# Performance work log

Hardware: AMD Instinct MI355X
Metric: run time of the kernel (lower is better)

## Reference

```python
import jax, jax.numpy as jnp
import numpy as np

B, TIN, IN, TRI, D, FFN, L, OUT = 8, 1040, 80, 128, 512, 2048, 8, 1024
H, DH, STRIDE, SEG, RC, LC, MAXMEM = 8, 64, 4, 16, 4, 32, 4
NEG = -1e8
SCALE = DH ** -0.5


def _layer_norm(x, g, b, eps=1e-5):
    m = jnp.mean(x, -1, keepdims=True)
    v = jnp.var(x, -1, keepdims=True)
    return (x - m) * jax.lax.rsqrt(v + eps) * g + b


def _build_attention_mask(U, nseg):
    # Faithful port of Emformer._gen_attention_mask; True = masked out.
    rct = RC * nseg
    mlen = nseg - 1
    rc_rows, q_rows, s_rows = [], [], []
    for i in range(nseg):
        rs, re = i * RC, i * RC + RC
        ss, se = max(i * SEG - LC, 0), min((i + 1) * SEG, U)
        ms = max(i - MAXMEM, 0)
        widths = [ms, i - ms, mlen - i, rs, RC, rct - re, ss, se - ss, U - se]

        def row(allowed):
            return np.concatenate([np.full(max(w, 0), j in allowed, dtype=bool)
                                   for j, w in enumerate(widths)])

        r = row({1, 4, 7})  # memory, own rc block, own (left-extended) segment
        rc_rows.append(np.tile(r, (RC, 1)))
        q_rows.append(np.tile(r, (min(SEG, U - i * SEG), 1)))
        s_rows.append(row({4, 7})[None])  # summary: rc block + segment only
    allow = np.concatenate([np.concatenate(rc_rows), np.concatenate(q_rows), np.concatenate(s_rows)])
    return jnp.asarray(~allow)


def _forward(input, lengths, w_in, ln_in_g, ln_in_b, wq, bq, wk, bk, wv, bv, wo, bo,
             ff_ln_g, ff_ln_b, w1, b1, w2, b2, ln_out_g, ln_out_b, w_out, b_out, lng, lnb):
    x = input @ w_in                                    # (B, TIN, TRI) input_linear (no bias)
    nb, t, _ = x.shape
    nf = t - t % STRIDE
    x = x[:, :nf].reshape(nb, nf // STRIDE, TRI * STRIDE)  # time reduction -> (B, Tr, D)
    lr = lengths // STRIDE
    x = jnp.transpose(x, (1, 0, 2))                     # (Tr, B, D) time-major like torch Emformer
    Tr = x.shape[0]
    U = Tr - RC                                         # utterance length (256)
    nseg = -(-U // SEG)
    utt = x[:U]
    # right-context blocks: hard-copied per segment (last block = trailing rc)
    starts = np.concatenate([np.arange(1, nseg) * SEG, [Tr - RC]])
    idx = (starts[:, None] + np.arange(RC)[None, :]).reshape(-1)
    rc = x[idx]                                         # (nseg*RC, B, D)
    Rt = rc.shape[0]
    Q = Rt + U + nseg                                   # rc + utterance + summary queries
    K = (nseg - 1) + Rt + U                             # mems + rc + utterance keys
    attn_mask = _build_attention_mask(U, nseg)          # (Q, K)
    mems0 = utt.reshape(nseg, SEG, nb, D).mean(1)[:-1]  # AvgPool1d(seg) on raw utterance, drop last
    # padding mask over keys (faithful to _gen_padding_mask)
    rcbl = Q - jnp.max(lr) - nseg
    klen = lr + (nseg - 1) + rcbl
    pad = jnp.arange(K)[None, :] >= klen[:, None]       # (B, K), True = masked

    def step(carry, p):
        utt, rc, mems = carry
        g1, be1, Wq, Bq, Wk, Bk, Wv, Bv, Wo, Bo, g2, be2, Wf1, Bf1, Wf2, Bf2, g3, be3 = p
        ln = _layer_norm(jnp.concatenate([rc, utt]), g1, be1)
        ln_rc, ln_utt = ln[:Rt], ln[Rt:]
        summary = ln_utt.reshape(nseg, SEG, nb, D).mean(1)       # (nseg, B, D)
        qin = jnp.concatenate([ln_rc, ln_utt, summary])          # (Q, B, D)
        kin = jnp.concatenate([mems, ln_rc, ln_utt])             # (K, B, D)
        q = (qin @ Wq + Bq).reshape(Q, nb, H, DH)
        k = (kin @ Wk + Bk).reshape(K, nb, H, DH)
        v = (kin @ Wv + Bv).reshape(K, nb, H, DH)
        w = jnp.einsum('qbhd,kbhd->bhqk', q * SCALE, k)
        w = jnp.where(attn_mask[None, None], NEG, w)
        w = jnp.where(pad[:, None, None, :], NEG, w)
        probs = jax.nn.softmax(w, axis=-1)
        att = jnp.einsum('bhqk,kbhd->qbhd', probs, v).reshape(Q, nb, D)
        out = att @ Wo + Bo
        rcu = out[:Rt + U]
        new_mems = jnp.tanh(out[Rt + U:])[:-1]                   # tanh_on_mem=True, drop last summary
        res = rcu + jnp.concatenate([rc, utt])                   # residual w/ pre-LN input
        h = _layer_norm(res, g2, be2)
        h = jax.nn.relu(h @ Wf1 + Bf1) @ Wf2 + Bf2               # pos_ff (pre-LN inside)
        res = res + h
        res = _layer_norm(res, g3, be3)
        return (res[Rt:], res[:Rt], new_mems), None

    xs = (ln_in_g, ln_in_b, wq, bq, wk, bk, wv, bv, wo, bo,
          ff_ln_g, ff_ln_b, w1, b1, w2, b2, ln_out_g, ln_out_b)
    (utt, rc, mems), _ = jax.lax.scan(step, (utt, rc, mems0), xs)
    y = jnp.transpose(utt, (1, 0, 2))                   # (B, U, D)
    y = _layer_norm(y @ w_out + b_out, lng, lnb)        # output_linear + LayerNorm
    return y, lr


def setup_inputs() -> dict:
    key = jax.random.key(0)
    ks = jax.random.split(key, 12)

    def w(k, shape, fan):
        return jax.random.normal(k, shape, jnp.float32) / np.sqrt(fan)

    return {
        "input": jax.random.normal(ks[0], (B, TIN, IN), jnp.float32),
        "lengths": jax.random.randint(ks[1], (B,), 256, 1025, jnp.int32),
        "w_in": w(ks[2], (IN, TRI), IN),
        "ln_in_g": jnp.ones((L, D), jnp.float32), "ln_in_b": jnp.zeros((L, D), jnp.float32),
        "wq": w(ks[3], (L, D, D), D), "bq": jnp.zeros((L, D), jnp.float32),
        "wk": w(ks[4], (L, D, D), D), "bk": jnp.zeros((L, D), jnp.float32),
        "wv": w(ks[5], (L, D, D), D), "bv": jnp.zeros((L, D), jnp.float32),
        "wo": w(ks[6], (L, D, D), D), "bo": jnp.zeros((L, D), jnp.float32),
        "ff_ln_g": jnp.ones((L, D), jnp.float32), "ff_ln_b": jnp.zeros((L, D), jnp.float32),
        "w1": w(ks[7], (L, D, FFN), D), "b1": jnp.zeros((L, FFN), jnp.float32),
        "w2": w(ks[8], (L, FFN, D), FFN), "b2": jnp.zeros((L, D), jnp.float32),
        "ln_out_g": jnp.ones((L, D), jnp.float32), "ln_out_b": jnp.zeros((L, D), jnp.float32),
        "w_out": w(ks[9], (D, OUT), D), "b_out": jnp.zeros((OUT,), jnp.float32),
        "lng": jnp.ones((OUT,), jnp.float32), "lnb": jnp.zeros((OUT,), jnp.float32),
    }


def reference(input, lengths, w_in, ln_in_g, ln_in_b, wq, bq, wk, bk, wv, bv, wo, bo,
              ff_ln_g, ff_ln_b, w1, b1, w2, b2, ln_out_g, ln_out_b, w_out, b_out, lng, lnb):
    return _forward(input, lengths, w_in, ln_in_g, ln_in_b, wq, bq, wk, bk, wv, bv, wo, bo,
                    ff_ln_g, ff_ln_b, w1, b1, w2, b2, ln_out_g, ln_out_b, w_out, b_out, lng, lnb)
```

## Files before the change

### kernel.cpp

```cpp
#include <hip/hip_runtime.h>
#include <math.h>

#define NB 8
#define D 512
#define H 8
#define DH 64
#define NSEG 16
#define RT 64
#define UU 256
#define QN 336
#define KN 335
#define SROWS 320
#define FFN_D 2048
#define LAYERS 8
#define OUTD 1024
#define TR 260
#define NEGV (-100000000.0f)
#define QSCALE 0.125f

typedef __attribute__((ext_vector_type(8))) short bf16x8;
typedef __attribute__((ext_vector_type(4))) float f32x4;

__device__ inline unsigned short f2bf(float f) {
    union { float f; unsigned int u; } v; v.f = f;
    unsigned int u = v.u;
    unsigned int r = (u + 0x7FFFu + ((u >> 16) & 1u)) >> 16;
    return (unsigned short)r;
}
__device__ inline float bf2f(unsigned short h) {
    union { unsigned int u; float f; } v; v.u = ((unsigned int)h) << 16;
    return v.f;
}

__global__ void lr_k(const int* __restrict__ lengths, int* __restrict__ lrw,
                     float* __restrict__ out_lr) {
    if (threadIdx.x == 0) {
        int mx = 0;
        for (int b = 0; b < NB; ++b) {
            int v = lengths[b] >> 2;
            lrw[b] = v;
            out_lr[b] = (float)v;
            if (v > mx) mx = v;
        }
        lrw[NB] = mx;
    }
}

__global__ __launch_bounds__(128) void inproj_k(const float* __restrict__ input,
                                                const float* __restrict__ w_in,
                                                float* __restrict__ XB) {
    __shared__ float wl[80 * 128];
    __shared__ float il[4 * 80];
    int tid = threadIdx.x;
    int t = blockIdx.x >> 3;
    int b = blockIdx.x & 7;
    for (int i = tid; i < 80 * 128; i += 128) wl[i] = w_in[i];
    const float* inp = input + ((size_t)b * 1040 + (size_t)t * 4) * 80;
    for (int i = tid; i < 320; i += 128) il[i] = inp[i];
    __syncthreads();
    float* xrow = XB + ((size_t)(t * NB + b)) * D;
#pragma unroll
    for (int c = 0; c < 4; ++c) {
        float acc = 0.f;
        for (int i = 0; i < 80; ++i) acc = fmaf(il[c * 80 + i], wl[i * 128 + tid], acc);
        xrow[c * 128 + tid] = acc;
    }
}

__global__ __launch_bounds__(256) void initstate_k(const float* __restrict__ XB,
                                                   float* __restrict__ S) {
    int r = blockIdx.x;
    int srow = r >> 3, b = r & 7;
    int src;
    if (srow < RT) {
        int i = srow >> 2, jj = srow & 3;
        src = (i < 15 ? (i + 1) * 16 : 256) + jj;
    } else {
        src = srow - RT;
    }
    const float* xr = XB + ((size_t)(src * NB + b)) * D;
    float* sr = S + (size_t)r * D;
    sr[threadIdx.x] = xr[threadIdx.x];
    sr[threadIdx.x + 256] = xr[threadIdx.x + 256];
}

__global__ __launch_bounds__(256) void mems0_k(const float* __restrict__ XB,
                                               unsigned short* __restrict__ MEMS) {
    int ib = blockIdx.x;
    int i = ib >> 3, b = ib & 7;
    for (int c = 0; c < 2; ++c) {
        int col = threadIdx.x + c * 256;
        float s = 0.f;
#pragma unroll
        for (int t = 0; t < 16; ++t) s += XB[((size_t)((i * 16 + t) * NB + b)) * D + col];
        MEMS[(size_t)ib * D + col] = f2bf(s * (1.f / 16.f));
    }
}

__global__ __launch_bounds__(256) void ln_k(const float* __restrict__ X,
                                            unsigned short* __restrict__ Y16,
                                            float* __restrict__ Yf,
                                            const float* __restrict__ g,
                                            const float* __restrict__ be, int dual) {
    int row = blockIdx.x;
    const float* x = X + (size_t)row * D;
    float v[2];
    float s = 0.f, ss = 0.f;
#pragma unroll
    for (int j = 0; j < 2; ++j) {
        v[j] = x[threadIdx.x + j * 256];
        s += v[j];
        ss = fmaf(v[j], v[j], ss);
    }
#pragma unroll
    for (int off = 32; off; off >>= 1) {
        s += __shfl_xor(s, off);
        ss += __shfl_xor(ss, off);
    }
    __shared__ float rs_[4], rss_[4];
    int w = threadIdx.x >> 6;
    if ((threadIdx.x & 63) == 0) {
        rs_[w] = s;
        rss_[w] = ss;
    }
    __syncthreads();
    s = rs_[0] + rs_[1] + rs_[2] + rs_[3];
    ss = rss_[0] + rss_[1] + rss_[2] + rss_[3];
    float mean = s * (1.f / D);
    float var = ss * (1.f / D) - mean * mean;
    float rstd = rsqrtf(var + 1e-5f);
#pragma unroll
    for (int j = 0; j < 2; ++j) {
        int col = threadIdx.x + j * 256;
        float y = (v[j] - mean) * rstd * g[col] + be[col];
        Y16[(size_t)row * D + col] = f2bf(y);
        if (dual) Yf[(size_t)row * D + col] = y;
    }
}

__global__ __launch_bounds__(256) void ln_res_k(const float* __restrict__ OUTB,
                                                float* __restrict__ SB,
                                                unsigned short* __restrict__ MEMS,
                                                unsigned short* __restrict__ Y16,
                                                const float* __restrict__ g,
                                                const float* __restrict__ be) {
    int row = blockIdx.x;
    if (row >= SROWS * NB) {
        int j = row - SROWS * NB;
#pragma unroll
        for (int c = 0; c < 2; ++c) {
            int col = threadIdx.x + c * 256;
            MEMS[(size_t)j * D + col] = f2bf(tanhf(OUTB[(size_t)row * D + col]));
        }
        return;
    }
    float v[2];
    float s = 0.f, ss = 0.f;
#pragma unroll
    for (int j = 0; j < 2; ++j) {
        int col = threadIdx.x + j * 256;
        float r = SB[(size_t)row * D + col] + OUTB[(size_t)row * D + col];
        SB[(size_t)row * D + col] = r;
        v[j] = r;
        s += r;
        ss = fmaf(r, r, ss);
    }
#pragma unroll
    for (int off = 32; off; off >>= 1) {
        s += __shfl_xor(s, off);
        ss += __shfl_xor(ss, off);
    }
    __shared__ float rs_[4], rss_[4];
    int w = threadIdx.x >> 6;
    if ((threadIdx.x & 63) == 0) {
        rs_[w] = s;
        rss_[w] = ss;
    }
    __syncthreads();
    s = rs_[0] + rs_[1] + rs_[2] + rs_[3];
    ss = rss_[0] + rss_[1] + rss_[2] + rss_[3];
    float mean = s * (1.f / D);
    float var = ss * (1.f / D) - mean * mean;
    float rstd = rsqrtf(var + 1e-5f);
#pragma unroll
    for (int j = 0; j < 2; ++j) {
        int col = threadIdx.x + j * 256;
        Y16[(size_t)row * D + col] = f2bf((v[j] - mean) * rstd * g[col] + be[col]);
    }
}

__global__ __launch_bounds__(256) void summary_k(const unsigned short* __restrict__ LN16,
                                                 unsigned short* __restrict__ SUM16) {
    int ib = blockIdx.x;
    int i = ib >> 3, b = ib & 7;
    for (int c = 0; c < 2; ++c) {
        int col = threadIdx.x + c * 256;
        float s = 0.f;
#pragma unroll
        for (int t = 0; t < 16; ++t)
            s += bf2f(LN16[((size_t)((RT + i * 16 + t) * NB + b)) * D + col]);
        SUM16[(size_t)ib * D + col] = f2bf(s * (1.f / 16.f));
    }
}

__device__ inline void conv_tile(float (*tile)[33], const float* __restrict__ src, int srcN,
                                 int k0, int sn0, unsigned short* __restrict__ dst, int dstK,
                                 int dn0) {
    int t = threadIdx.x;
    int r = t >> 3, c4 = (t & 7) * 4;
    float4 v = *(const float4*)&src[(size_t)(k0 + r) * srcN + sn0 + c4];
    tile[r][c4 + 0] = v.x;
    tile[r][c4 + 1] = v.y;
    tile[r][c4 + 2] = v.z;
    tile[r][c4 + 3] = v.w;
    __syncthreads();
    ushort4 o;
    o.x = f2bf(tile[c4 + 0][r]);
    o.y = f2bf(tile[c4 + 1][r]);
    o.z = f2bf(tile[c4 + 2][r]);
    o.w = f2bf(tile[c4 + 3][r]);
    *(ushort4*)&dst[(size_t)(dn0 + r) * dstK + k0 + c4] = o;
}

__global__ __launch_bounds__(256) void convw_k(const float* __restrict__ wq,
                                               const float* __restrict__ wk,
                                               const float* __restrict__ wv,
                                               const float* __restrict__ wo,
                                               const float* __restrict__ w1,
                                               const float* __restrict__ w2,
                                               const float* __restrict__ bq,
                                               const float* __restrict__ bk,
                                               const float* __restrict__ bv,
                                               unsigned short* __restrict__ WQKV,
                                               unsigned short* __restrict__ WO16,
                                               unsigned short* __restrict__ W1T,
                                               unsigned short* __restrict__ W2T,
                                               float* __restrict__ BQKV, int l) {
    __shared__ float tile[32][33];
    int t = blockIdx.x;
    if (t == 0) {
        for (int i = threadIdx.x; i < 1536; i += 256)
            BQKV[i] = i < 512 ? bq[l * 512 + i]
                              : (i < 1024 ? bk[l * 512 + i - 512] : bv[l * 512 + i - 1024]);
    }
    if (t < 768) {
        int tn = t % 48, tk = t / 48;
        int n0 = tn * 32, k0 = tk * 32;
        const float* src;
        int sn0;
        if (n0 < 512) { src = wq + (size_t)l * 262144; sn0 = n0; }
        else if (n0 < 1024) { src = wk + (size_t)l * 262144; sn0 = n0 - 512; }
        else { src = wv + (size_t)l * 262144; sn0 = n0 - 1024; }
        conv_tile(tile, src, 512, k0, sn0, WQKV, 512, n0);
    } else if (t < 1024) {
        int tt = t - 768;
        int n0 = (tt % 16) * 32, k0 = (tt / 16) * 32;
        conv_tile(tile, wo + (size_t)l * 262144, 512, k0, n0, WO16, 512, n0);
    } else if (t < 2048) {
        int tt = t - 1024;
        int n0 = (tt % 64) * 32, k0 = (tt / 64) * 32;
        conv_tile(tile, w1 + (size_t)l * 1048576, 2048, k0, n0, W1T, 512, n0);
    } else {
        int tt = t - 2048;
        int n0 = (tt % 16) * 32, k0 = (tt / 16) * 32;
        conv_tile(tile, w2 + (size_t)l * 1048576, 512, k0, n0, W2T, 2048, n0);
    }
}

__global__ __launch_bounds__(256) void convout_k(const float* __restrict__ w_out,
                                                 unsigned short* __restrict__ WOUT16) {
    __shared__ float tile[32][33];
    int t = blockIdx.x;
    int n0 = (t % 32) * 32, k0 = (t / 32) * 32;
    conv_tile(tile, w_out, 1024, k0, n0, WOUT16, 512, n0);
}

__global__ __launch_bounds__(256) void gemm16_k(const unsigned short* __restrict__ A,
                                                const unsigned short* __restrict__ BT,
                                                const float* __restrict__ bias,
                                                void* __restrict__ Cp, int M, int N, int K,
                                                int Kchunk, int flags) {
    __shared__ unsigned short As[2][64][40];
    __shared__ unsigned short Bs[2][64][40];
    int tid = threadIdx.x;
    int wave = tid >> 6, lane = tid & 63;
    int wm = wave >> 1, wn = wave & 1;
    int quad = lane >> 4, sub = lane & 15;
    int m0 = blockIdx.y * 64, n0 = blockIdx.x * 64;
    int kb = blockIdx.z * Kchunk, ke = kb + Kchunk;

    int lrow = tid >> 3, lkc = tid & 7;
    int lrow2 = lrow + 32;
    int lkh = lkc >> 2, lkl = lkc & 3;

    f32x4 acc[2][2] = {};
    int4 ar0, ar1, br0, br1;

    auto loadT = [&](int k0) {
        int gr0 = m0 + lrow, gr1 = m0 + lrow2;
        ar0 = (gr0 < M) ? *(const int4*)&A[(size_t)gr0 * K + k0 + lkc * 8] : make_int4(0, 0, 0, 0);
        ar1 = (gr1 < M) ? *(const int4*)&A[(size_t)gr1 * K + k0 + lkc * 8] : make_int4(0, 0, 0, 0);
        br0 = *(const int4*)&BT[(size_t)(n0 + lrow) * K + k0 + lkc * 8];
        br1 = *(const int4*)&BT[(size_t)(n0 + lrow2) * K + k0 + lkc * 8];
    };
    auto storeT = [&]() {
        *(int4*)&As[lkh][lrow][lkl * 8] = ar0;
        *(int4*)&As[lkh][lrow2][lkl * 8] = ar1;
        *(int4*)&Bs[lkh][lrow][lkl * 8] = br0;
        *(int4*)&Bs[lkh][lrow2][lkl * 8] = br1;
    };
    auto compute = [&]() {
#pragma unroll
        for (int ks = 0; ks < 2; ++ks) {
            bf16x8 af[2], bf[2];
#pragma unroll
            for (int mi = 0; mi < 2; ++mi)
                af[mi] = *(const bf16x8*)&As[ks][wm * 32 + mi * 16 + sub][quad * 8];
#pragma unroll
            for (int ni = 0; ni < 2; ++ni)
                bf[ni] = *(const bf16x8*)&Bs[ks][wn * 32 + ni * 16 + sub][quad * 8];
#pragma unroll
            for (int mi = 0; mi < 2; ++mi)
#pragma unroll
                for (int ni = 0; ni < 2; ++ni)
                    acc[mi][ni] = __builtin_amdgcn_mfma_f32_16x16x32_bf16(af[mi], bf[ni],
                                                                          acc[mi][ni], 0, 0, 0);
        }
    };

    loadT(kb);
    storeT();
    __syncthreads();
    for (int k0 = kb + 64; k0 < ke; k0 += 64) {
        loadT(k0);
        compute();
        __syncthreads();
        storeT();
        __syncthreads();
    }
    compute();

    bool relu = flags & 1, addc = flags & 2, obf = flags & 4, atom = flags & 8;
    bool addbias = !atom || blockIdx.z == 0;
    float* Cf = (float*)Cp;
    unsigned short* Ch = (unsigned short*)Cp;
#pragma unroll
    for (int mi = 0; mi < 2; ++mi) {
#pragma unroll
        for (int ni = 0; ni < 2; ++ni) {
#pragma unroll
            for (int r = 0; r < 4; ++r) {
                int row = m0 + wm * 32 + mi * 16 + quad * 4 + r;
                int col = n0 + wn * 32 + ni * 16 + sub;
                if (row < M) {
                    float v = acc[mi][ni][r] + (addbias ? bias[col] : 0.f);
                    if (relu) v = fmaxf(v, 0.f);
                    size_t idx = (size_t)row * N + col;
                    if (obf) {
                        Ch[idx] = f2bf(v);
                    } else if (atom) {
                        atomicAdd(&Cf[idx], v);
                    } else {
                        if (addc) v += Cf[idx];
                        Cf[idx] = v;
                    }
                }
            }
        }
    }
}

__global__ __launch_bounds__(256) void attn_k(const unsigned short* __restrict__ QKV,
                                              unsigned short* __restrict__ ATT,
                                              const int* __restrict__ lrw) {
    int tid = threadIdx.x;
    int qrow = blockIdx.x;
    int b = blockIdx.y;

    int i, is_sum;
    if (qrow < RT) {
        i = qrow >> 2;
        is_sum = 0;
    } else if (qrow < RT + UU) {
        i = (qrow - RT) >> 4;
        is_sum = 0;
    } else {
        i = qrow - (RT + UU);
        is_sum = 1;
    }
    int ms = (i > 4) ? (i - 4) : 0;
    int n_mem = is_sum ? 0 : (i - ms);
    int us = (i * 16 - 32 > 0) ? (i * 16 - 32) : 0;
    int ue = (i + 1) * 16;
    int total = n_mem + 4 + (ue - us);
    int klen = KN + lrw[b] - lrw[NB];

    __shared__ float qs[512];
    __shared__ float sc[H][64];
    __shared__ int kks[64];

    {
        const unsigned int* qrp =
            (const unsigned int*)&QKV[(size_t)(120 + qrow * NB + b) * 1536];
        unsigned int u = qrp[tid];
        qs[2 * tid] = __uint_as_float(u << 16) * QSCALE;
        qs[2 * tid + 1] = __uint_as_float(u & 0xFFFF0000u) * QSCALE;
    }
    if (tid < 64) {
        int kk = -1;
        if (tid < total) {
            if (tid < n_mem)
                kk = ms + tid;
            else if (tid < n_mem + 4)
                kk = 15 + i * 4 + (tid - n_mem);
            else
                kk = 79 + us + (tid - n_mem - 4);
        }
        kks[tid] = kk;
    }
    __syncthreads();

#pragma unroll
    for (int rep = 0; rep < 2; ++rep) {
        int p = rep * 256 + tid;
        int h = p >> 6, j = p & 63;
        int kk = kks[j];
        float s = NEGV;
        if (kk >= 0 && kk < klen) {
            const int4* kr = (const int4*)&QKV[(size_t)(kk * NB + b) * 1536 + 512 + h * DH];
            const float* qh = &qs[h * DH];
            float accd = 0.f;
#pragma unroll
            for (int c = 0; c < 8; ++c) {
                int4 kv = kr[c];
                const int uu[4] = {kv.x, kv.y, kv.z, kv.w};
#pragma unroll
                for (int jj = 0; jj < 4; ++jj) {
                    float lo = __uint_as_float(((unsigned)uu[jj]) << 16);
                    float hi = __uint_as_float(((unsigned)uu[jj]) & 0xFFFF0000u);
                    accd = fmaf(lo, qh[c * 8 + jj * 2], accd);
                    accd = fmaf(hi, qh[c * 8 + jj * 2 + 1], accd);
                }
            }
            s = accd;
        }
        sc[h][j] = s;
    }
    __syncthreads();

    {
        int wv = tid >> 6, lane = tid & 63;
#pragma unroll
        for (int hh = 0; hh < 2; ++hh) {
            int h = wv + hh * 4;
            float s = sc[h][lane];
            float m = s;
#pragma unroll
            for (int off = 32; off; off >>= 1) m = fmaxf(m, __shfl_xor(m, off));
            float p = __expf(s - m);
            float sum = p;
#pragma unroll
            for (int off = 32; off; off >>= 1) sum += __shfl_xor(sum, off);
            sc[h][lane] = p / sum;
        }
    }
    __syncthreads();

    {
        int h = tid >> 5;
        const float* ph = sc[h];
        float a0 = 0.f, a1 = 0.f;
        const unsigned short* vbase = QKV + (size_t)b * 1536 + 1024 + 2 * tid;
#pragma unroll 4
        for (int j = 0; j < total; ++j) {
            int kkj = kks[j];
            unsigned int u = *(const unsigned int*)&vbase[(size_t)kkj * (NB * 1536)];
            float p = ph[j];
            a0 = fmaf(p, __uint_as_float(u << 16), a0);
            a1 = fmaf(p, __uint_as_float(u & 0xFFFF0000u), a1);
        }
        unsigned int o = ((unsigned int)f2bf(a0)) | (((unsigned int)f2bf(a1)) << 16);
        *(unsigned int*)&ATT[(size_t)(qrow * NB + b) * D + 2 * tid] = o;
    }
}

__global__ __launch_bounds__(256) void final_ln_k(const float* __restrict__ Yb,
                                                  const float* __restrict__ g,
                                                  const float* __restrict__ be,
                                                  float* __restrict__ out) {
    int row = blockIdx.x;
    int u = row >> 3, b = row & 7;
    const float* x = Yb + (size_t)row * OUTD;
    float v[4];
    float s = 0.f, ss = 0.f;
#pragma unroll
    for (int j = 0; j < 4; ++j) {
        v[j] = x[threadIdx.x + j * 256];
        s += v[j];
        ss = fmaf(v[j], v[j], ss);
    }
#pragma unroll
    for (int off = 32; off; off >>= 1) {
        s += __shfl_xor(s, off);
        ss += __shfl_xor(ss, off);
    }
    __shared__ float rs_[4], rss_[4];
    int w = threadIdx.x >> 6;
    if ((threadIdx.x & 63) == 0) {
        rs_[w] = s;
        rss_[w] = ss;
    }
    __syncthreads();
    s = rs_[0] + rs_[1] + rs_[2] + rs_[3];
    ss = rss_[0] + rss_[1] + rss_[2] + rss_[3];
    float mean = s * (1.f / OUTD);
    float var = ss * (1.f / OUTD) - mean * mean;
    float rstd = rsqrtf(var + 1e-5f);
    float* o = out + ((size_t)(b * 256 + u)) * OUTD;
#pragma unroll
    for (int j = 0; j < 4; ++j) {
        int col = threadIdx.x + j * 256;
        o[col] = (v[j] - mean) * rstd * g[col] + be[col];
    }
}

extern "C" void kernel_launch(void* const* d_in, const int* in_sizes, int n_in, void* d_out,
                              int out_size, void* d_ws, size_t ws_size, hipStream_t stream) {
    (void)in_sizes;
    (void)n_in;
    (void)out_size;
    (void)ws_size;
    const float* input = (const float*)d_in[0];
    const int* lengths = (const int*)d_in[1];
    const float* w_in = (const float*)d_in[2];
    const float* ln_in_g = (const float*)d_in[3];
    const float* ln_in_b = (const float*)d_in[4];
    const float* wq = (const float*)d_in[5];
    const float* bq = (const float*)d_in[6];
    const float* wk = (const float*)d_in[7];
    const float* bk = (const float*)d_in[8];
    const float* wv = (const float*)d_in[9];
    const float* bv = (const float*)d_in[10];
    const float* wo = (const float*)d_in[11];
    const float* bo = (const float*)d_in[12];
    const float* ff_g = (const float*)d_in[13];
    const float* ff_b = (const float*)d_in[14];
    const float* w1 = (const float*)d_in[15];
    const float* b1 = (const float*)d_in[16];
    const float* w2 = (const float*)d_in[17];
    const float* b2 = (const float*)d_in[18];
    const float* lo_g = (const float*)d_in[19];
    const float* lo_b = (const float*)d_in[20];
    const float* w_out = (const float*)d_in[21];
    const float* b_out = (const float*)d_in[22];
    const float* lng = (const float*)d_in[23];
    const float* lnb = (const float*)d_in[24];
    float* out = (float*)d_out;

    char* wsc = (char*)d_ws;
    size_t off = 0;
    auto alloc = [&](size_t bytes) {
        char* p = wsc + off;
        off += (bytes + 255) & ~(size_t)255;
        return p;
    };
    unsigned short* ACT16 = (unsigned short*)alloc(2808ULL * 512 * 2);
    unsigned short* ATT16 = (unsigned short*)alloc(2688ULL * 512 * 2);
    unsigned short* HB16 = (unsigned short*)alloc(2560ULL * 2048 * 2);
    unsigned short* QKVB = (unsigned short*)alloc(2808ULL * 1536 * 2);
    float* SB = (float*)alloc(2560ULL * 512 * 4);
    unsigned short* WQKV16 = (unsigned short*)alloc(1536ULL * 512 * 2);
    unsigned short* WO16 = (unsigned short*)alloc(512ULL * 512 * 2);
    unsigned short* W1T = (unsigned short*)alloc(2048ULL * 512 * 2);
    unsigned short* W2T = (unsigned short*)alloc(512ULL * 2048 * 2);
    unsigned short* WOUT16 = (unsigned short*)alloc(1024ULL * 512 * 2);
    float* BQKV = (float*)alloc(1536 * 4);
    int* LRW = (int*)alloc(64);

    unsigned short* MEMS16 = ACT16;
    unsigned short* LNB16 = ACT16 + 120 * 512;
    unsigned short* SUMB16 = ACT16 + 2680 * 512;
    float* XB = (float*)QKVB;
    float* OUTB = (float*)QKVB;
    float* HBf = (float*)QKVB;

    lr_k<<<1, 64, 0, stream>>>(lengths, LRW, out + (size_t)NB * 256 * 1024);
    convout_k<<<512, 256, 0, stream>>>(w_out, WOUT16);
    inproj_k<<<TR * NB, 128, 0, stream>>>(input, w_in, XB);
    initstate_k<<<SROWS * NB, 256, 0, stream>>>(XB, SB);
    mems0_k<<<15 * NB, 256, 0, stream>>>(XB, MEMS16);

    for (int l = 0; l < LAYERS; ++l) {
        convw_k<<<3072, 256, 0, stream>>>(wq, wk, wv, wo, w1, w2, bq, bk, bv, WQKV16, WO16, W1T,
                                          W2T, BQKV, l);
        ln_k<<<SROWS * NB, 256, 0, stream>>>(SB, LNB16, SB, ln_in_g + l * D, ln_in_b + l * D, 0);
        summary_k<<<NSEG * NB, 256, 0, stream>>>(LNB16, SUMB16);
        gemm16_k<<<dim3(24, 44, 1), 256, 0, stream>>>(ACT16, WQKV16, BQKV, QKVB, 2808, 1536, 512,
                                                      512, 4);
        attn_k<<<dim3(QN, NB), 256, 0, stream>>>(QKVB, ATT16, LRW);
        gemm16_k<<<dim3(8, 42, 1), 256, 0, stream>>>(ATT16, WO16, bo + l * D, OUTB, QN * NB, D,
                                                     D, D, 0);
        ln_res_k<<<(SROWS + 15) * NB, 256, 0, stream>>>(OUTB, SB, MEMS16, LNB16, ff_g + l * D,
                                                        ff_b + l * D);
        gemm16_k<<<dim3(32, 40, 1), 256, 0, stream>>>(LNB16, W1T, b1 + l * FFN_D, HB16,
                                                      SROWS * NB, FFN_D, D, D, 1 | 4);
        gemm16_k<<<dim3(8, 40, 4), 256, 0, stream>>>(HB16, W2T, b2 + l * D, SB, SROWS * NB, D,
                                                     FFN_D, 512, 8);
        ln_k<<<SROWS * NB, 256, 0, stream>>>(SB, LNB16, SB, lo_g + l * D, lo_b + l * D, 1);
    }
    gemm16_k<<<dim3(16, 32, 1), 256, 0, stream>>>(LNB16 + (size_t)RT * NB * D, WOUT16, b_out,
                                                  HBf, UU * NB, OUTD, D, D, 0);
    final_ln_k<<<UU * NB, 256, 0, stream>>>(HBf, lng, lnb, out);
}
```

Measured before the change: 1.196 ms.

## Convert all layer weights in one launch and use async LDS loads in GEMM

Moves the per-layer bf16 weight conversion out of the layer loop into a single launch that converts every layer's weights plus the output projection into per-layer buffers, which removes eight serialized conversion launches. The GEMM kernel now copies its A and B tiles straight from global memory into LDS with global_load_lds, into an XOR-swizzled single buffer that avoids bank conflicts. This drops the register-staged double buffer, so global loads no longer overlap the MFMA work, and the row bounds check on A is gone. Out-of-range rows (2808 is not a multiple of 64) now read past the end of the A buffer, and the workspace grows to hold all layers' converted weights.

```diff
diff --git a/kernel.cpp b/kernel.cpp
--- a/kernel.cpp
+++ b/kernel.cpp
@@ -32,6 +32,11 @@
     return v.f;
 }
 
+__device__ inline void async16(const void* g, void* l) {
+    __builtin_amdgcn_global_load_lds((const __attribute__((address_space(1))) void*)g,
+                                     (__attribute__((address_space(3))) void*)l, 16, 0, 0);
+}
+
 __global__ void lr_k(const int* __restrict__ lengths, int* __restrict__ lrw,
                      float* __restrict__ out_lr) {
     if (threadIdx.x == 0) {
@@ -222,26 +227,36 @@
     *(ushort4*)&dst[(size_t)(dn0 + r) * dstK + k0 + c4] = o;
 }
 
-__global__ __launch_bounds__(256) void convw_k(const float* __restrict__ wq,
-                                               const float* __restrict__ wk,
-                                               const float* __restrict__ wv,
-                                               const float* __restrict__ wo,
-                                               const float* __restrict__ w1,
-                                               const float* __restrict__ w2,
-                                               const float* __restrict__ bq,
-                                               const float* __restrict__ bk,
-                                               const float* __restrict__ bv,
-                                               unsigned short* __restrict__ WQKV,
-                                               unsigned short* __restrict__ WO16,
-                                               unsigned short* __restrict__ W1T,
-                                               unsigned short* __restrict__ W2T,
-                                               float* __restrict__ BQKV, int l) {
+__global__ __launch_bounds__(256) void convw_all_k(const float* __restrict__ wq,
+                                                   const float* __restrict__ wk,
+                                                   const float* __restrict__ wv,
+                                                   const float* __restrict__ wo,
+                                                   const float* __restrict__ w1,
+                                                   const float* __restrict__ w2,
+                                                   const float* __restrict__ bq,
+                                                   const float* __restrict__ bk,
+                                                   const float* __restrict__ bv,
+                                                   const float* __restrict__ w_out,
+                                                   unsigned short* __restrict__ WQKV,
+                                                   unsigned short* __restrict__ WO16,
+                                                   unsigned short* __restrict__ W1T,
+                                                   unsigned short* __restrict__ W2T,
+                                                   unsigned short* __restrict__ WOUT16,
+                                                   float* __restrict__ BQKV) {
     __shared__ float tile[32][33];
-    int t = blockIdx.x;
+    int tb = blockIdx.x;
+    if (tb >= LAYERS * 3072) {
+        int t = tb - LAYERS * 3072;
+        int n0 = (t % 32) * 32, k0 = (t / 32) * 32;
+        conv_tile(tile, w_out, 1024, k0, n0, WOUT16, 512, n0);
+        return;
+    }
+    int l = tb / 3072, t = tb % 3072;
     if (t == 0) {
         for (int i = threadIdx.x; i < 1536; i += 256)
-            BQKV[i] = i < 512 ? bq[l * 512 + i]
-                              : (i < 1024 ? bk[l * 512 + i - 512] : bv[l * 512 + i - 1024]);
+            BQKV[l * 1536 + i] = i < 512 ? bq[l * 512 + i]
+                                         : (i < 1024 ? bk[l * 512 + i - 512]
+                                                     : bv[l * 512 + i - 1024]);
     }
     if (t < 768) {
         int tn = t % 48, tk = t / 48;
@@ -251,28 +266,23 @@
         if (n0 < 512) { src = wq + (size_t)l * 262144; sn0 = n0; }
         else if (n0 < 1024) { src = wk + (size_t)l * 262144; sn0 = n0 - 512; }
         else { src = wv + (size_t)l * 262144; sn0 = n0 - 1024; }
-        conv_tile(tile, src, 512, k0, sn0, WQKV, 512, n0);
+        conv_tile(tile, src, 512, k0, sn0, WQKV + (size_t)l * 1536 * 512, 512, n0);
     } else if (t < 1024) {
         int tt = t - 768;
         int n0 = (tt % 16) * 32, k0 = (tt / 16) * 32;
-        conv_tile(tile, wo + (size_t)l * 262144, 512, k0, n0, WO16, 512, n0);
+        conv_tile(tile, wo + (size_t)l * 262144, 512, k0, n0, WO16 + (size_t)l * 512 * 512, 512,
+                  n0);
     } else if (t < 2048) {
         int tt = t - 1024;
         int n0 = (tt % 64) * 32, k0 = (tt / 64) * 32;
-        conv_tile(tile, w1 + (size_t)l * 1048576, 2048, k0, n0, W1T, 512, n0);
+        conv_tile(tile, w1 + (size_t)l * 1048576, 2048, k0, n0, W1T + (size_t)l * 2048 * 512, 512,
+                  n0);
     } else {
         int tt = t - 2048;
         int n0 = (tt % 16) * 32, k0 = (tt / 16) * 32;
-        conv_tile(tile, w2 + (size_t)l * 1048576, 512, k0, n0, W2T, 2048, n0);
-    }
-}
-
-__global__ __launch_bounds__(256) void convout_k(const float* __restrict__ w_out,
-                                                 unsigned short* __restrict__ WOUT16) {
-    __shared__ float tile[32][33];
-    int t = blockIdx.x;
-    int n0 = (t % 32) * 32, k0 = (t / 32) * 32;
-    conv_tile(tile, w_out, 1024, k0, n0, WOUT16, 512, n0);
+        conv_tile(tile, w2 + (size_t)l * 1048576, 512, k0, n0, W2T + (size_t)l * 512 * 2048, 2048,
+                  n0);
+    }
 }
 
 __global__ __launch_bounds__(256) void gemm16_k(const unsigned short* __restrict__ A,
@@ -280,8 +290,8 @@
                                                 const float* __restrict__ bias,
                                                 void* __restrict__ Cp, int M, int N, int K,
                                                 int Kchunk, int flags) {
-    __shared__ unsigned short As[2][64][40];
-    __shared__ unsigned short Bs[2][64][40];
+    __shared__ unsigned short As[64 * 64];
+    __shared__ unsigned short Bs[64 * 64];
     int tid = threadIdx.x;
     int wave = tid >> 6, lane = tid & 63;
     int wm = wave >> 1, wn = wave & 1;
@@ -289,56 +299,44 @@
     int m0 = blockIdx.y * 64, n0 = blockIdx.x * 64;
     int kb = blockIdx.z * Kchunk, ke = kb + Kchunk;
 
-    int lrow = tid >> 3, lkc = tid & 7;
-    int lrow2 = lrow + 32;
-    int lkh = lkc >> 2, lkl = lkc & 3;
+    int s0 = wave * 128 + lane;
+    int s1 = s0 + 64;
+    int r0 = s0 >> 3, c0 = (s0 & 7) ^ (r0 & 7);
+    int r1 = s1 >> 3, c1 = (s1 & 7) ^ (r1 & 7);
+    const unsigned short* gA0 = A + (size_t)(m0 + r0) * K + c0 * 8 + kb;
+    const unsigned short* gA1 = A + (size_t)(m0 + r1) * K + c1 * 8 + kb;
+    const unsigned short* gB0 = BT + (size_t)(n0 + r0) * K + c0 * 8 + kb;
+    const unsigned short* gB1 = BT + (size_t)(n0 + r1) * K + c1 * 8 + kb;
+    unsigned short* lA0 = &As[(wave * 128) * 8];
+    unsigned short* lA1 = &As[(wave * 128 + 64) * 8];
+    unsigned short* lB0 = &Bs[(wave * 128) * 8];
+    unsigned short* lB1 = &Bs[(wave * 128 + 64) * 8];
+
+    int rowA0 = wm * 32 + sub, rowA1 = rowA0 + 16;
+    int rowB0 = wn * 32 + sub, rowB1 = rowB0 + 16;
 
     f32x4 acc[2][2] = {};
-    int4 ar0, ar1, br0, br1;
-
-    auto loadT = [&](int k0) {
-        int gr0 = m0 + lrow, gr1 = m0 + lrow2;
-        ar0 = (gr0 < M) ? *(const int4*)&A[(size_t)gr0 * K + k0 + lkc * 8] : make_int4(0, 0, 0, 0);
-        ar1 = (gr1 < M) ? *(const int4*)&A[(size_t)gr1 * K + k0 + lkc * 8] : make_int4(0, 0, 0, 0);
-        br0 = *(const int4*)&BT[(size_t)(n0 + lrow) * K + k0 + lkc * 8];
-        br1 = *(const int4*)&BT[(size_t)(n0 + lrow2) * K + k0 + lkc * 8];
-    };
-    auto storeT = [&]() {
-        *(int4*)&As[lkh][lrow][lkl * 8] = ar0;
-        *(int4*)&As[lkh][lrow2][lkl * 8] = ar1;
-        *(int4*)&Bs[lkh][lrow][lkl * 8] = br0;
-        *(int4*)&Bs[lkh][lrow2][lkl * 8] = br1;
-    };
-    auto compute = [&]() {
+    for (int k0 = 0; k0 < Kchunk; k0 += 64) {
+        async16(gA0 + k0, lA0);
+        async16(gA1 + k0, lA1);
+        async16(gB0 + k0, lB0);
+        async16(gB1 + k0, lB1);
+        __syncthreads();
 #pragma unroll
         for (int ks = 0; ks < 2; ++ks) {
-            bf16x8 af[2], bf[2];
-#pragma unroll
-            for (int mi = 0; mi < 2; ++mi)
-                af[mi] = *(const bf16x8*)&As[ks][wm * 32 + mi * 16 + sub][quad * 8];
-#pragma unroll
-            for (int ni = 0; ni < 2; ++ni)
-                bf[ni] = *(const bf16x8*)&Bs[ks][wn * 32 + ni * 16 + sub][quad * 8];
-#pragma unroll
-            for (int mi = 0; mi < 2; ++mi)
-#pragma unroll
-                for (int ni = 0; ni < 2; ++ni)
-                    acc[mi][ni] = __builtin_amdgcn_mfma_f32_16x16x32_bf16(af[mi], bf[ni],
-                                                                          acc[mi][ni], 0, 0, 0);
-        }
-    };
-
-    loadT(kb);
-    storeT();
-    __syncthreads();
-    for (int k0 = kb + 64; k0 < ke; k0 += 64) {
-        loadT(k0);
-        compute();
+            int cc = ks * 4 + quad;
+            bf16x8 af0 = *(const bf16x8*)&As[rowA0 * 64 + ((cc ^ (rowA0 & 7)) * 8)];
+            bf16x8 af1 = *(const bf16x8*)&As[rowA1 * 64 + ((cc ^ (rowA1 & 7)) * 8)];
+            bf16x8 bf0 = *(const bf16x8*)&Bs[rowB0 * 64 + ((cc ^ (rowB0 & 7)) * 8)];
+            bf16x8 bf1 = *(const bf16x8*)&Bs[rowB1 * 64 + ((cc ^ (rowB1 & 7)) * 8)];
+            acc[0][0] = __builtin_amdgcn_mfma_f32_16x16x32_bf16(af0, bf0, acc[0][0], 0, 0, 0);
+            acc[0][1] = __builtin_amdgcn_mfma_f32_16x16x32_bf16(af0, bf1, acc[0][1], 0, 0, 0);
+            acc[1][0] = __builtin_amdgcn_mfma_f32_16x16x32_bf16(af1, bf0, acc[1][0], 0, 0, 0);
+            acc[1][1] = __builtin_amdgcn_mfma_f32_16x16x32_bf16(af1, bf1, acc[1][1], 0, 0, 0);
+        }
         __syncthreads();
-        storeT();
-        __syncthreads();
-    }
-    compute();
+    }
+    (void)ke;
 
     bool relu = flags & 1, addc = flags & 2, obf = flags & 4, atom = flags & 8;
     bool addbias = !atom || blockIdx.z == 0;
@@ -569,12 +567,12 @@
     unsigned short* HB16 = (unsigned short*)alloc(2560ULL * 2048 * 2);
     unsigned short* QKVB = (unsigned short*)alloc(2808ULL * 1536 * 2);
     float* SB = (float*)alloc(2560ULL * 512 * 4);
-    unsigned short* WQKV16 = (unsigned short*)alloc(1536ULL * 512 * 2);
-    unsigned short* WO16 = (unsigned short*)alloc(512ULL * 512 * 2);
-    unsigned short* W1T = (unsigned short*)alloc(2048ULL * 512 * 2);
-    unsigned short* W2T = (unsigned short*)alloc(512ULL * 2048 * 2);
+    unsigned short* WQKV16 = (unsigned short*)alloc(8ULL * 1536 * 512 * 2);
+    unsigned short* WO16 = (unsigned short*)alloc(8ULL * 512 * 512 * 2);
+    unsigned short* W1T = (unsigned short*)alloc(8ULL * 2048 * 512 * 2);
+    unsigned short* W2T = (unsigned short*)alloc(8ULL * 512 * 2048 * 2);
     unsigned short* WOUT16 = (unsigned short*)alloc(1024ULL * 512 * 2);
-    float* BQKV = (float*)alloc(1536 * 4);
+    float* BQKV = (float*)alloc(8ULL * 1536 * 4);
     int* LRW = (int*)alloc(64);
 
     unsigned short* MEMS16 = ACT16;
@@ -585,30 +583,33 @@
     float* HBf = (float*)QKVB;
 
     lr_k<<<1, 64, 0, stream>>>(lengths, LRW, out + (size_t)NB * 256 * 1024);
-    convout_k<<<512, 256, 0, stream>>>(w_out, WOUT16);
+    convw_all_k<<<LAYERS * 3072 + 512, 256, 0, stream>>>(wq, wk, wv, wo, w1, w2, bq, bk, bv,
+                                                         w_out, WQKV16, WO16, W1T, W2T, WOUT16,
+                                                         BQKV);
     inproj_k<<<TR * NB, 128, 0, stream>>>(input, w_in, XB);
     initstate_k<<<SROWS * NB, 256, 0, stream>>>(XB, SB);
     mems0_k<<<15 * NB, 256, 0, stream>>>(XB, MEMS16);
 
     for (int l = 0; l < LAYERS; ++l) {
-        convw_k<<<3072, 256, 0, stream>>>(wq, wk, wv, wo, w1, w2, bq, bk, bv, WQKV16, WO16, W1T,
-                                          W2T, BQKV, l);
         ln_k<<<SROWS * NB, 256, 0, stream>>>(SB, LNB16, SB, ln_in_g + l * D, ln_in_b + l * D, 0);
         summary_k<<<NSEG * NB, 256, 0, stream>>>(LNB16, SUMB16);
-        gemm16_k<<<dim3(24, 44, 1), 256, 0, stream>>>(ACT16, WQKV16, BQKV, QKVB, 2808, 1536, 512,
-                                                      512, 4);
+        gemm16_k<<<dim3(24, 44, 1), 256, 0, stream>>>(ACT16, WQKV16 + (size_t)l * 1536 * 512,
+                                                      BQKV + l * 1536, QKVB, 2808, 1536, 512, 512,
+                                                      4);
         attn_k<<<dim3(QN, NB), 256, 0, stream>>>(QKVB, ATT16, LRW);
-        gemm16_k<<<dim3(8, 42, 1), 256, 0, stream>>>(ATT16, WO16, bo + l * D, OUTB, QN * NB, D,
-                                                     D, D, 0);
+        gemm16_k<<<dim3(8, 42, 1), 256, 0, stream>>>(ATT16, WO16 + (size_t)l * 512 * 512,
+                                                     bo + l * D, OUTB, QN * NB, D, D, 512, 0);
         ln_res_k<<<(SROWS + 15) * NB, 256, 0, stream>>>(OUTB, SB, MEMS16, LNB16, ff_g + l * D,
                                                         ff_b + l * D);
-        gemm16_k<<<dim3(32, 40, 1), 256, 0, stream>>>(LNB16, W1T, b1 + l * FFN_D, HB16,
-                                                      SROWS * NB, FFN_D, D, D, 1 | 4);
-        gemm16_k<<<dim3(8, 40, 4), 256, 0, stream>>>(HB16, W2T, b2 + l * D, SB, SROWS * NB, D,
-                                                     FFN_D, 512, 8);
+        gemm16_k<<<dim3(32, 40, 1), 256, 0, stream>>>(LNB16, W1T + (size_t)l * 2048 * 512,
+                                                      b1 + l * FFN_D, HB16, SROWS * NB, FFN_D,
+                                                      512, 512, 1 | 4);
+        gemm16_k<<<dim3(8, 40, 4), 256, 0, stream>>>(HB16, W2T + (size_t)l * 512 * 2048,
+                                                     b2 + l * D, SB, SROWS * NB, D, FFN_D, 512,
+                                                     8);
         ln_k<<<SROWS * NB, 256, 0, stream>>>(SB, LNB16, SB, lo_g + l * D, lo_b + l * D, 1);
     }
     gemm16_k<<<dim3(16, 32, 1), 256, 0, stream>>>(LNB16 + (size_t)RT * NB * D, WOUT16, b_out,
-                                                  HBf, UU * NB, OUTD, D, D, 0);
+                                                  HBf, UU * NB, OUTD, 512, 512, 0);
     final_ln_k<<<UU * NB, 256, 0, stream>>>(HBf, lng, lnb, out);
 }
```

New measurement: 1.113 ms. -6.9%, faster.
